# Kernel tuning notes

Measured on AMD Instinct MI355X. Metric: run time of the kernel, lower is better.

Reference implementation:

```python
import jax, jax.numpy as jnp
import numpy as np

N = 2048   # atoms (m == n from einsum structure)
F = 64     # dist_exp_size
H = 128    # atom_emb_size
K = 256    # hidden_size


def setup_inputs() -> dict:
    key = jax.random.key(0)
    k1, k2, k3, k4, k5 = jax.random.split(key, 5)
    dist_adj = jax.random.uniform(k1, (N, N), dtype=jnp.float32)
    dist_exp = jax.random.normal(k2, (N, N, F), dtype=jnp.float32)
    atom_emb = jax.random.normal(k3, (N, H), dtype=jnp.float32)
    # parameters: torch.rand -> uniform [0,1)
    bilinear_w = jax.random.uniform(k4, (F, H, K), dtype=jnp.float32)
    bilinear_b = jax.random.uniform(k5, (K,), dtype=jnp.float32)
    return {"dist_adj": dist_adj, "dist_exp": dist_exp, "atom_emb": atom_emb,
            "bilinear_w": bilinear_w, "bilinear_b": bilinear_b}


def reference(dist_adj, dist_exp, atom_emb, bilinear_w, bilinear_b):
    # adjacency-weighted aggregation over neighbors: [n, f]
    adj_exp = jnp.einsum('mn,mnf->mf', dist_adj, dist_exp)
    # trilinear bilinear contraction per node: [n, k]
    feat = jnp.einsum('nf,fhk,nh->nk', adj_exp, bilinear_w, atom_emb)
    # softplus activation, then bias added AFTER activation (faithful to source)
    return jax.nn.softplus(feat) + bilinear_b
```

## Files before the change

### kernel.cpp

```cpp
#include <hip/hip_runtime.h>
#include <hip/hip_bf16.h>

#define N_ATOMS 2048
#define F_DIM   64
#define H_DIM   128
#define K_DIM   256
#define KD      8192
#define BM 32
#define BN 64
#define BK 128
#define NT (KD / BK)

typedef __attribute__((ext_vector_type(8))) short short8;
typedef __attribute__((ext_vector_type(4))) float f32x4;
typedef __attribute__((ext_vector_type(8))) unsigned short ushort8v;

static __device__ __forceinline__ unsigned short f2bf(float x) {
  unsigned int u = __float_as_uint(x);
  u += 0x7fff + ((u >> 16) & 1);
  return (unsigned short)(u >> 16);
}

__global__ __launch_bounds__(256) void fused_prep_kernel(
    const float* __restrict__ dist_adj,
    const float* __restrict__ dist_exp,
    const float* __restrict__ W,
    float* __restrict__ adj_exp,
    unsigned short* __restrict__ Wt) {
  __shared__ __align__(16) char smem[17408];
  const int t = threadIdx.x;

  if (blockIdx.x < 512) {
    const int q    = blockIdx.x;
    const int cb   = q >> 7;
    const int kb   = (q >> 1) & 63;
    const int half = q & 1;
    float (*tile)[68] = (float(*)[68])smem;

    {
      const int r0 = t >> 4;
      const int c4 = (t & 15) * 4;
      #pragma unroll
      for (int i = 0; i < 4; ++i) {
        const int r = i * 16 + r0;
        f32x4 v = *(const f32x4*)(W + (size_t)(kb * 128 + half * 64 + r) * K_DIM + cb * 64 + c4);
        tile[r][c4 + 0] = v[0]; tile[r][c4 + 1] = v[1];
        tile[r][c4 + 2] = v[2]; tile[r][c4 + 3] = v[3];
      }
    }
    __syncthreads();
    {
      char* outb = (char*)Wt + (size_t)((cb << 6) | kb) * 16384;
      #pragma unroll
      for (int j = 0; j < 2; ++j) {
        const int lin  = t * 32 + j * 16;
        const int cc   = lin >> 7;
        const int w128 = lin & 127;
        const int k0   = (w128 ^ ((cc & 7) << 4)) >> 1;
        ushort8v v;
        #pragma unroll
        for (int e = 0; e < 8; ++e) v[e] = f2bf(tile[k0 + e][cc]);
        *(ushort8v*)(outb + cc * 256 + half * 128 + w128) = v;
      }
    }
  } else {
    const int m  = blockIdx.x - 512;
    const int f4 = t & 15;
    const int ng = t >> 4;

    float* arowl = (float*)smem;
    f32x4* red   = (f32x4*)(smem + 8192);

    {
      const f32x4* src = (const f32x4*)(dist_adj + (size_t)m * N_ATOMS);
      f32x4* dst = (f32x4*)arowl;
      #pragma unroll
      for (int i = 0; i < 2; ++i) {
        const int idx = i * 256 + t;
        dst[idx] = __builtin_nontemporal_load(src + idx);
      }
    }
    __syncthreads();

    const float* __restrict__ base = dist_exp + (size_t)m * N_ATOMS * F_DIM + f4 * 4;
    f32x4 acc = {0.f, 0.f, 0.f, 0.f};
    #pragma unroll 4
    for (int n = ng; n < N_ATOMS; n += 16) {
      float a  = arowl[n];
      f32x4 v = __builtin_nontemporal_load((const f32x4*)(base + (size_t)n * F_DIM));
      acc += a * v;
    }

    red[ng * 16 + f4] = acc;
    __syncthreads();
    if (t < 16) {
      f32x4 s = red[t];
      #pragma unroll
      for (int g = 1; g < 16; ++g) s += red[g * 16 + t];
      *(f32x4*)(adj_exp + m * F_DIM + t * 4) = s;
    }
  }
}

__global__ __launch_bounds__(256) void bilinear_kernel(
    const float* __restrict__ adj_exp,
    const float* __restrict__ emb,
    const unsigned short* __restrict__ Wt,
    const float* __restrict__ bias,
    float* __restrict__ out) {
  const int b  = blockIdx.x;
  const int wg = (b & 7) * 32 + (b >> 3);
  const int mb = wg & 63;
  const int cb = wg >> 6;
  const int m0 = mb * BM;
  const int c0 = cb * BN;

  const int t  = threadIdx.x;
  const int w  = t >> 6;
  const int l  = t & 63;
  const int lr = l & 15;
  const int lg = l >> 4;

  __shared__ __align__(16) unsigned short Bl[2][8192];
  __shared__ __align__(16) float adjT[F_DIM][BM];

  const char* wt_base = (const char*)Wt;
  #define STAGE_B(buf, step)                                                      \
    {                                                                             \
      const char* src = wt_base + (size_t)((cb << 6) | (step)) * 16384;           \
      char* dstb = (char*)&Bl[(buf)][0];                                          \
      _Pragma("unroll")                                                           \
      for (int i = 0; i < 4; ++i) {                                               \
        const int chunk = i * 4 + w;                                              \
        __builtin_amdgcn_global_load_lds(                                         \
            (const __attribute__((address_space(1))) unsigned int*)(src + chunk * 1024 + l * 16), \
            (__attribute__((address_space(3))) unsigned int*)(dstb + chunk * 1024), \
            16, 0, 0);                                                            \
      }                                                                           \
    }

  STAGE_B(0, 0);

  short8 Ef0[4], Ef1[4];
  #pragma unroll
  for (int ks = 0; ks < 4; ++ks) {
    const float* p0 = emb + (size_t)(m0 + lr) * H_DIM + ks * 32 + lg * 8;
    const float* p1 = emb + (size_t)(m0 + 16 + lr) * H_DIM + ks * 32 + lg * 8;
    f32x4 u0 = *(const f32x4*)p0, u1 = *(const f32x4*)(p0 + 4);
    f32x4 v0 = *(const f32x4*)p1, v1 = *(const f32x4*)(p1 + 4);
    short8 e0, e1;
    #pragma unroll
    for (int i = 0; i < 4; ++i) {
      e0[i]     = (short)f2bf(u0[i]); e0[4 + i] = (short)f2bf(u1[i]);
      e1[i]     = (short)f2bf(v0[i]); e1[4 + i] = (short)f2bf(v1[i]);
    }
    Ef0[ks] = e0; Ef1[ks] = e1;
  }
  {
    const int r  = t & 31;
    const int f0 = (t >> 5) * 8;
    f32x4 a0 = *(const f32x4*)(adj_exp + (size_t)(m0 + r) * F_DIM + f0);
    f32x4 a1 = *(const f32x4*)(adj_exp + (size_t)(m0 + r) * F_DIM + f0 + 4);
    adjT[f0 + 0][r] = a0[0]; adjT[f0 + 1][r] = a0[1];
    adjT[f0 + 2][r] = a0[2]; adjT[f0 + 3][r] = a0[3];
    adjT[f0 + 4][r] = a1[0]; adjT[f0 + 5][r] = a1[1];
    adjT[f0 + 6][r] = a1[2]; adjT[f0 + 7][r] = a1[3];
  }
  __syncthreads();

  f32x4 facc0 = {0.f, 0.f, 0.f, 0.f};
  f32x4 facc1 = {0.f, 0.f, 0.f, 0.f};
  const int ccol = w * 16 + lr;
  const int bswz = (lr & 7) << 4;

  int cur = 0;
  #pragma unroll 1
  for (int ts = 0; ts < NT; ++ts) {
    const int nxt = cur ^ 1;
    if (ts + 1 < NT) {
      STAGE_B(nxt, ts + 1);
      asm volatile("s_waitcnt vmcnt(4)" ::: "memory");
    } else {
      asm volatile("s_waitcnt vmcnt(0)" ::: "memory");
    }
    __builtin_amdgcn_s_barrier();
    asm volatile("" ::: "memory");

    f32x4 a0 = *(const f32x4*)&adjT[ts][lg * 4];
    f32x4 a1 = *(const f32x4*)&adjT[ts][16 + lg * 4];

    const char* Bbase = (const char*)&Bl[cur][0];
    f32x4 t0 = {0.f, 0.f, 0.f, 0.f};
    f32x4 t1 = {0.f, 0.f, 0.f, 0.f};
    #pragma unroll
    for (int ks = 0; ks < 4; ++ks) {
      const int boff = ccol * 256 + ((ks * 64 + lg * 16) ^ bswz);
      short8 bf = *(const short8*)(Bbase + boff);
      t0 = __builtin_amdgcn_mfma_f32_16x16x32_bf16(Ef0[ks], bf, t0, 0, 0, 0);
      t1 = __builtin_amdgcn_mfma_f32_16x16x32_bf16(Ef1[ks], bf, t1, 0, 0, 0);
    }
    facc0 += a0 * t0;
    facc1 += a1 * t1;

    asm volatile("s_waitcnt lgkmcnt(0)" ::: "memory");
    __builtin_amdgcn_s_barrier();
    asm volatile("" ::: "memory");
    cur = nxt;
  }
  #undef STAGE_B

  const int col = c0 + ccol;
  const float bb = bias[col];
  #pragma unroll
  for (int r = 0; r < 4; ++r) {
    const int row0 = m0 + lg * 4 + r;
    float x0  = facc0[r];
    float sp0 = (x0 > 20.f) ? x0 : ((x0 < -20.f) ? __expf(x0) : log1pf(__expf(x0)));
    out[(size_t)row0 * K_DIM + col] = sp0 + bb;
    const int row1 = row0 + 16;
    float x1  = facc1[r];
    float sp1 = (x1 > 20.f) ? x1 : ((x1 < -20.f) ? __expf(x1) : log1pf(__expf(x1)));
    out[(size_t)row1 * K_DIM + col] = sp1 + bb;
  }
}

extern "C" void kernel_launch(void* const* d_in, const int* in_sizes, int n_in,
                              void* d_out, int out_size, void* d_ws, size_t ws_size,
                              hipStream_t stream) {
  const float* dist_adj   = (const float*)d_in[0];
  const float* dist_exp   = (const float*)d_in[1];
  const float* atom_emb   = (const float*)d_in[2];
  const float* bilinear_w = (const float*)d_in[3];
  const float* bilinear_b = (const float*)d_in[4];
  float* out = (float*)d_out;

  float* adj_exp = (float*)d_ws;
  unsigned short* Wt =
      (unsigned short*)((char*)d_ws + (size_t)N_ATOMS * F_DIM * sizeof(float));

  hipLaunchKernelGGL(fused_prep_kernel, dim3(512 + N_ATOMS), dim3(256), 0, stream,
                     dist_adj, dist_exp, bilinear_w, adj_exp, Wt);
  hipLaunchKernelGGL(bilinear_kernel, dim3((N_ATOMS / BM) * (K_DIM / BN)), dim3(256), 0, stream,
                     adj_exp, atom_emb, Wt, bilinear_b, out);
}
```

Before: 225.5 us.

## Retile bilinear GEMM to 64x32 blocks with 4-stage LDS ring and one barrier

Changes the bilinear kernel tile from 32 rows x 64 columns to 64 rows x 32 columns, with each wave covering a 32x16 sub-tile. The prep kernel now writes Wt in 8 KB chunks per 32-column group to match. The LDS buffer becomes a 4-deep ring with a prefetch distance of two, which removes the second barrier and the lgkmcnt wait per K step. Each W tile is now loaded by half as many blocks worth of columns but reused across more rows, cutting W traffic per output. The risk is a thinner per-step stage and reliance on the ring depth to avoid write-after-read hazards without the trailing barrier.

```diff
diff --git a/kernel.cpp b/kernel.cpp
--- a/kernel.cpp
+++ b/kernel.cpp
@@ -6,8 +6,8 @@
 #define H_DIM   128
 #define K_DIM   256
 #define KD      8192
-#define BM 32
-#define BN 64
+#define BM 64
+#define BN 32
 #define BK 128
 #define NT (KD / BK)
 
@@ -50,7 +50,7 @@
     }
     __syncthreads();
     {
-      char* outb = (char*)Wt + (size_t)((cb << 6) | kb) * 16384;
+      char* outb = (char*)Wt;
       #pragma unroll
       for (int j = 0; j < 2; ++j) {
         const int lin  = t * 32 + j * 16;
@@ -60,7 +60,8 @@
         ushort8v v;
         #pragma unroll
         for (int e = 0; e < 8; ++e) v[e] = f2bf(tile[k0 + e][cc]);
-        *(ushort8v*)(outb + cc * 256 + half * 128 + w128) = v;
+        const size_t tb = (size_t)(((cb * 2 + (cc >> 5)) << 6) | kb) * 8192;
+        *(ushort8v*)(outb + tb + (cc & 31) * 256 + half * 128 + w128) = v;
       }
     }
   } else {
@@ -108,30 +109,32 @@
     const unsigned short* __restrict__ Wt,
     const float* __restrict__ bias,
     float* __restrict__ out) {
-  const int b  = blockIdx.x;
-  const int wg = (b & 7) * 32 + (b >> 3);
-  const int mb = wg & 63;
-  const int cb = wg >> 6;
-  const int m0 = mb * BM;
-  const int c0 = cb * BN;
+  const int b   = blockIdx.x;
+  const int wg  = (b & 7) * 32 + (b >> 3);
+  const int cbt = wg >> 5;
+  const int mb  = wg & 31;
+  const int m0  = mb * BM;
+  const int c0  = cbt * BN;
 
   const int t  = threadIdx.x;
   const int w  = t >> 6;
   const int l  = t & 63;
   const int lr = l & 15;
   const int lg = l >> 4;
-
-  __shared__ __align__(16) unsigned short Bl[2][8192];
+  const int cg = w & 1;
+  const int rb = (w >> 1) * 32;
+
+  __shared__ __align__(16) unsigned short Bl[4][4096];
   __shared__ __align__(16) float adjT[F_DIM][BM];
 
   const char* wt_base = (const char*)Wt;
   #define STAGE_B(buf, step)                                                      \
     {                                                                             \
-      const char* src = wt_base + (size_t)((cb << 6) | (step)) * 16384;           \
+      const char* src = wt_base + (size_t)((cbt << 6) | (step)) * 8192;           \
       char* dstb = (char*)&Bl[(buf)][0];                                          \
       _Pragma("unroll")                                                           \
-      for (int i = 0; i < 4; ++i) {                                               \
-        const int chunk = i * 4 + w;                                              \
+      for (int i = 0; i < 2; ++i) {                                               \
+        const int chunk = w * 2 + i;                                              \
         __builtin_amdgcn_global_load_lds(                                         \
             (const __attribute__((address_space(1))) unsigned int*)(src + chunk * 1024 + l * 16), \
             (__attribute__((address_space(3))) unsigned int*)(dstb + chunk * 1024), \
@@ -140,80 +143,79 @@
     }
 
   STAGE_B(0, 0);
+  STAGE_B(1, 1);
 
   short8 Ef0[4], Ef1[4];
-  #pragma unroll
-  for (int ks = 0; ks < 4; ++ks) {
-    const float* p0 = emb + (size_t)(m0 + lr) * H_DIM + ks * 32 + lg * 8;
-    const float* p1 = emb + (size_t)(m0 + 16 + lr) * H_DIM + ks * 32 + lg * 8;
-    f32x4 u0 = *(const f32x4*)p0, u1 = *(const f32x4*)(p0 + 4);
-    f32x4 v0 = *(const f32x4*)p1, v1 = *(const f32x4*)(p1 + 4);
-    short8 e0, e1;
+  {
+    const float* p0 = emb + (size_t)(m0 + rb + lr) * H_DIM;
+    const float* p1 = emb + (size_t)(m0 + rb + 16 + lr) * H_DIM;
+    #pragma unroll
+    for (int ks = 0; ks < 4; ++ks) {
+      f32x4 u0 = *(const f32x4*)(p0 + ks * 32 + lg * 8);
+      f32x4 u1 = *(const f32x4*)(p0 + ks * 32 + lg * 8 + 4);
+      f32x4 v0 = *(const f32x4*)(p1 + ks * 32 + lg * 8);
+      f32x4 v1 = *(const f32x4*)(p1 + ks * 32 + lg * 8 + 4);
+      short8 e0, e1;
+      #pragma unroll
+      for (int i = 0; i < 4; ++i) {
+        e0[i] = (short)f2bf(u0[i]); e0[4 + i] = (short)f2bf(u1[i]);
+        e1[i] = (short)f2bf(v0[i]); e1[4 + i] = (short)f2bf(v1[i]);
+      }
+      Ef0[ks] = e0; Ef1[ks] = e1;
+    }
+  }
+  {
+    const int r  = t & 63;
+    const int fb = (t >> 6) * 16;
     #pragma unroll
     for (int i = 0; i < 4; ++i) {
-      e0[i]     = (short)f2bf(u0[i]); e0[4 + i] = (short)f2bf(u1[i]);
-      e1[i]     = (short)f2bf(v0[i]); e1[4 + i] = (short)f2bf(v1[i]);
-    }
-    Ef0[ks] = e0; Ef1[ks] = e1;
-  }
-  {
-    const int r  = t & 31;
-    const int f0 = (t >> 5) * 8;
-    f32x4 a0 = *(const f32x4*)(adj_exp + (size_t)(m0 + r) * F_DIM + f0);
-    f32x4 a1 = *(const f32x4*)(adj_exp + (size_t)(m0 + r) * F_DIM + f0 + 4);
-    adjT[f0 + 0][r] = a0[0]; adjT[f0 + 1][r] = a0[1];
-    adjT[f0 + 2][r] = a0[2]; adjT[f0 + 3][r] = a0[3];
-    adjT[f0 + 4][r] = a1[0]; adjT[f0 + 5][r] = a1[1];
-    adjT[f0 + 6][r] = a1[2]; adjT[f0 + 7][r] = a1[3];
+      f32x4 a = *(const f32x4*)(adj_exp + (size_t)(m0 + r) * F_DIM + fb + i * 4);
+      adjT[fb + i * 4 + 0][r] = a[0]; adjT[fb + i * 4 + 1][r] = a[1];
+      adjT[fb + i * 4 + 2][r] = a[2]; adjT[fb + i * 4 + 3][r] = a[3];
+    }
   }
   __syncthreads();
 
   f32x4 facc0 = {0.f, 0.f, 0.f, 0.f};
   f32x4 facc1 = {0.f, 0.f, 0.f, 0.f};
-  const int ccol = w * 16 + lr;
-  const int bswz = (lr & 7) << 4;
-
-  int cur = 0;
+  const int c_loc = cg * 16 + lr;
+  const int bswz  = (lr & 7) << 4;
+
   #pragma unroll 1
   for (int ts = 0; ts < NT; ++ts) {
-    const int nxt = cur ^ 1;
-    if (ts + 1 < NT) {
-      STAGE_B(nxt, ts + 1);
+    if (ts + 2 < NT) {
+      STAGE_B((ts + 2) & 3, ts + 2);
       asm volatile("s_waitcnt vmcnt(4)" ::: "memory");
+    } else if (ts + 2 == NT) {
+      asm volatile("s_waitcnt vmcnt(2)" ::: "memory");
     } else {
       asm volatile("s_waitcnt vmcnt(0)" ::: "memory");
     }
     __builtin_amdgcn_s_barrier();
     asm volatile("" ::: "memory");
 
-    f32x4 a0 = *(const f32x4*)&adjT[ts][lg * 4];
-    f32x4 a1 = *(const f32x4*)&adjT[ts][16 + lg * 4];
-
-    const char* Bbase = (const char*)&Bl[cur][0];
+    const char* Bbase = (const char*)&Bl[ts & 3][0];
     f32x4 t0 = {0.f, 0.f, 0.f, 0.f};
     f32x4 t1 = {0.f, 0.f, 0.f, 0.f};
     #pragma unroll
     for (int ks = 0; ks < 4; ++ks) {
-      const int boff = ccol * 256 + ((ks * 64 + lg * 16) ^ bswz);
+      const int boff = c_loc * 256 + ((ks * 64 + lg * 16) ^ bswz);
       short8 bf = *(const short8*)(Bbase + boff);
       t0 = __builtin_amdgcn_mfma_f32_16x16x32_bf16(Ef0[ks], bf, t0, 0, 0, 0);
       t1 = __builtin_amdgcn_mfma_f32_16x16x32_bf16(Ef1[ks], bf, t1, 0, 0, 0);
     }
+    f32x4 a0 = *(const f32x4*)&adjT[ts][rb + lg * 4];
+    f32x4 a1 = *(const f32x4*)&adjT[ts][rb + 16 + lg * 4];
     facc0 += a0 * t0;
     facc1 += a1 * t1;
-
-    asm volatile("s_waitcnt lgkmcnt(0)" ::: "memory");
-    __builtin_amdgcn_s_barrier();
-    asm volatile("" ::: "memory");
-    cur = nxt;
   }
   #undef STAGE_B
 
-  const int col = c0 + ccol;
+  const int col = c0 + c_loc;
   const float bb = bias[col];
   #pragma unroll
   for (int r = 0; r < 4; ++r) {
-    const int row0 = m0 + lg * 4 + r;
+    const int row0 = m0 + rb + lg * 4 + r;
     float x0  = facc0[r];
     float sp0 = (x0 > 20.f) ? x0 : ((x0 < -20.f) ? __expf(x0) : log1pf(__expf(x0)));
     out[(size_t)row0 * K_DIM + col] = sp0 + bb;
```

After: 213.7 us. -5.2%, faster.
